# Kernel tuning notes

Hardware: AMD Instinct MI355X
Metric: run time of the kernel (lower is better)

The kernel has to match this reference:

```python
import jax, jax.numpy as jnp
import numpy as np

B, C, X, Y, Z = 2, 4, 128, 128, 96
_BIG = 1e10  # effectively infinite squared distance (no background in line)


def _edt_sq_pass(f, axis):
    """One separable pass of the exact squared EDT along `axis`:
    g[i] = min_j f[j] + (i - j)^2  (Felzenszwalb lower envelope, brute-forced
    with lax.map so only O(rest) memory per step)."""
    f = jnp.moveaxis(f, axis, -1)  # (..., L)
    idx = jnp.arange(f.shape[-1], dtype=f.dtype)
    g = jax.lax.map(lambda i: jnp.min(f + (i - idx) ** 2, axis=-1), idx)  # (L, ...)
    return jnp.moveaxis(jnp.moveaxis(g, 0, -1), -1, axis)


def _edt(mask):
    """Exact Euclidean distance of True voxels to the nearest False voxel
    (matches scipy.ndimage.distance_transform_edt on a binary mask)."""
    f = jnp.where(mask, _BIG, 0.0).astype(jnp.float32)
    for ax in (-3, -2, -1):  # three spatial axes
        f = _edt_sq_pass(f, ax)
    return jnp.sqrt(f)


def _neighbor(m, axis, d):
    """Shift `m` by d along `axis` with edge replication (reflect border,
    as in skimage's grey erosion used by find_boundaries)."""
    axis = axis % m.ndim
    pw = [(1, 1) if i == axis else (0, 0) for i in range(m.ndim)]
    p = jnp.pad(m, pw, mode='edge')
    sl = [slice(None)] * m.ndim
    sl[axis] = slice(1 + d, p.shape[axis] - 1 + d)
    return p[tuple(sl)]


def _inner_boundary(m):
    """skimage find_boundaries(mode='inner', connectivity=1): foreground voxels
    with at least one background face-neighbor."""
    eroded = m
    for ax in (-3, -2, -1):
        eroded = eroded & _neighbor(m, ax, 1) & _neighbor(m, ax, -1)
    return m & ~eroded


def _compute_sdf(onehot):
    """Signed distance map per (batch, class): negdis - posdis, zero on the
    inner boundary; zero where the class is absent; channel 0 is skipped."""
    posdis = _edt(onehot)          # dist inside object to background
    negdis = _edt(~onehot)         # dist outside object to foreground
    sdf = jnp.where(_inner_boundary(onehot), 0.0, negdis - posdis)
    any_pos = jnp.any(onehot, axis=(2, 3, 4), keepdims=True)
    sdf = jnp.where(any_pos, sdf, 0.0)
    return sdf.at[:, 0].set(0.0)   # loop starts at c=1 in the original


def setup_inputs() -> dict:
    key = jax.random.key(0)
    k1, k2 = jax.random.split(key)
    net_output = jax.random.normal(k1, (B, C, X, Y, Z), dtype=jnp.float32)
    gt = jax.random.randint(k2, (B, 1, X, Y, Z), 0, C, dtype=jnp.int32)
    return {"net_output": net_output, "gt": gt}


def reference(net_output, gt):
    probs = jax.nn.softmax(net_output, axis=1)  # softmax_helper = softmax over class dim
    classes = jnp.arange(net_output.shape[1], dtype=gt.dtype).reshape(1, -1, 1, 1, 1)
    onehot = gt == classes  # scatter_(1, gt, 1) one-hot, bool (B,C,X,Y,Z)
    phi = _compute_sdf(onehot)
    # einsum('bcxyz,bcxyz->bcxyz') on foreground channels, then global mean
    return jnp.mean(probs[:, 1:] * phi[:, 1:])
```

## Files before the change

kernel.cpp:

```cpp
#include <hip/hip_runtime.h>
#include <hip/hip_fp16.h>
#include <math.h>

#define XD 128
#define YD 128
#define ZD 96
#define NV (XD*YD*ZD)
#define SXX (YD*ZD)
#define SENT 49152
#define SENTP 0xC000C000u
#define TW2 114
#define TDW (TW2/2)
#define TROWS 144
#define SCANB 192
#define PROBB 1024

__global__ __launch_bounds__(384) void k_scan_prob(const int* __restrict__ gt,
                                                   const float* __restrict__ net,
                                                   unsigned char* __restrict__ out,
                                                   __half2* __restrict__ probs,
                                                   int* __restrict__ flags,
                                                   int batch0) {
    const int bb  = blockIdx.y;
    const int myb = batch0 + bb;
    const int tid = threadIdx.x;

    if (blockIdx.x >= SCANB) {
        const int p = (blockIdx.x - SCANB) * 384 + tid;
        const int idx = p * 4;
        const float* nb = net + (size_t)myb * 4 * NV;
        float4 v0 = *(const float4*)(nb + idx);
        float4 v1 = *(const float4*)(nb + NV + idx);
        float4 v2 = *(const float4*)(nb + 2 * NV + idx);
        float4 v3 = *(const float4*)(nb + 3 * NV + idx);

        const float a0[4] = {v0.x, v0.y, v0.z, v0.w};
        const float a1[4] = {v1.x, v1.y, v1.z, v1.w};
        const float a2[4] = {v2.x, v2.y, v2.z, v2.w};
        const float a3[4] = {v3.x, v3.y, v3.z, v3.w};
        float p1[4], p2[4], p3[4];
#pragma unroll
        for (int j = 0; j < 4; ++j) {
            float mx = fmaxf(fmaxf(a0[j], a1[j]), fmaxf(a2[j], a3[j]));
            float e0 = __expf(a0[j] - mx);
            float e1 = __expf(a1[j] - mx);
            float e2 = __expf(a2[j] - mx);
            float e3 = __expf(a3[j] - mx);
            float iv = __frcp_rn(e0 + e1 + e2 + e3);
            p1[j] = e1 * iv; p2[j] = e2 * iv; p3[j] = e3 * iv;
        }
        probs[(size_t)(myb * 3 + 0) * (NV / 2) + 2 * p]     = __floats2half2_rn(p1[0], p1[1]);
        probs[(size_t)(myb * 3 + 0) * (NV / 2) + 2 * p + 1] = __floats2half2_rn(p1[2], p1[3]);
        probs[(size_t)(myb * 3 + 1) * (NV / 2) + 2 * p]     = __floats2half2_rn(p2[0], p2[1]);
        probs[(size_t)(myb * 3 + 1) * (NV / 2) + 2 * p + 1] = __floats2half2_rn(p2[2], p2[3]);
        probs[(size_t)(myb * 3 + 2) * (NV / 2) + 2 * p]     = __floats2half2_rn(p3[0], p3[1]);
        probs[(size_t)(myb * 3 + 2) * (NV / 2) + 2 * p + 1] = __floats2half2_rn(p3[2], p3[3]);
        return;
    }

    const int l   = tid & 63;
    const int w6  = tid >> 6;
    const int lq0 = blockIdx.x * 64;

    __shared__ unsigned char gtile[64 * 132];
    __shared__ int blkbits;
    if (tid == 0) blkbits = 0;

    int mybits = 0;
    const int* gp = gt + (size_t)myb * NV + lq0 + l;
    for (int j = w6; j < XD; j += 6) {
        int g = gp[(size_t)j * SXX];
        mybits |= 1 << g;
        gtile[l * 132 + j] = (unsigned char)g;
    }
#pragma unroll
    for (int off = 32; off; off >>= 1) mybits |= __shfl_xor(mybits, off);
    __syncthreads();
    if ((tid & 63) == 0) atomicOr(&blkbits, mybits);

    unsigned int D[32];
    {
        const unsigned int ci = (unsigned int)((w6 >> 1) + 1);
        const int s = w6 & 1;
        unsigned int G[32];
        const unsigned int* grow = (const unsigned int*)gtile + l * 33;
#pragma unroll
        for (int q = 0; q < 32; ++q) G[q] = grow[q];

        int cnt = 200;
#pragma unroll
        for (int q = 0; q < 32; ++q) {
            unsigned int u = G[q], dv = 0;
#pragma unroll
            for (int b = 0; b < 4; ++b) {
                unsigned int gv = (u >> (8 * b)) & 255u;
                bool zero = s ? (gv == ci) : (gv != ci);
                cnt = zero ? 0 : ((cnt < 200) ? cnt + 1 : 200);
                dv |= (unsigned int)cnt << (8 * b);
            }
            D[q] = dv;
        }
        cnt = 200;
#pragma unroll
        for (int q = 31; q >= 0; --q) {
            unsigned int u = G[q], dv = D[q];
#pragma unroll
            for (int b = 3; b >= 0; --b) {
                unsigned int gv = (u >> (8 * b)) & 255u;
                bool zero = s ? (gv == ci) : (gv != ci);
                cnt = zero ? 0 : ((cnt < 200) ? cnt + 1 : 200);
                unsigned int old = (dv >> (8 * b)) & 255u;
                unsigned int nbv = ((unsigned int)cnt < old) ? (unsigned int)cnt : old;
                dv = (dv & ~(255u << (8 * b))) | (nbv << (8 * b));
            }
            D[q] = dv;
        }
    }
    __syncthreads();
    if (tid == 0) atomicOr(&flags[myb], blkbits);

    {
        const int r = l & 3;
        unsigned char* ob = out + (size_t)(bb * 6 + w6) * NV + lq0 + (l & ~3);
#pragma unroll
        for (int q = 0; q < 32; ++q) {
            unsigned int A = D[q];
            unsigned int Bv = (unsigned int)__shfl_xor((int)A, 1);
            unsigned int t = (r & 1)
                ? __builtin_amdgcn_perm(A, Bv, 0x07030501u)
                : __builtin_amdgcn_perm(A, Bv, 0x02060004u);
            unsigned int Cv = (unsigned int)__shfl_xor((int)t, 2);
            unsigned int y = (r & 2)
                ? __builtin_amdgcn_perm(t, Cv, 0x07060302u)
                : __builtin_amdgcn_perm(t, Cv, 0x01000504u);
            *(unsigned int*)(ob + (size_t)(4 * q + r) * SXX) = y;
        }
    }
}

__device__ __forceinline__ unsigned int pk_min(unsigned int a, unsigned int b) {
    unsigned int d;
    asm("v_pk_min_u16 %0, %1, %2" : "=v"(d) : "v"(a), "v"(b));
    return d;
}
__device__ __forceinline__ unsigned int pk_max(unsigned int a, unsigned int b) {
    unsigned int d;
    asm("v_pk_max_u16 %0, %1, %2" : "=v"(d) : "v"(a), "v"(b));
    return d;
}
__device__ __forceinline__ unsigned int pk_add(unsigned int a, unsigned int b) {
    unsigned int d;
    asm("v_pk_add_u16 %0, %1, %2" : "=v"(d) : "v"(a), "v"(b));
    return d;
}

__device__ __forceinline__ bool pk_done(const unsigned int m[8], int thr) {
    unsigned int mx = m[0];
#pragma unroll
    for (int k = 1; k < 8; ++k) mx = pk_max(mx, m[k]);
    int a = (int)(mx & 0xFFFFu), bq = (int)(mx >> 16);
    int amax = a > bq ? a : bq;
    return __all(amax <= thr) != 0;
}

template<int STRIDE, int L>
__device__ __forceinline__ void edt_slow8(const unsigned short* __restrict__ p0,
                                          int i0, float m[8]) {
    int t = 9;
    bool done = false;
    while (!done && t < L) {
        for (int u = 0; u < 4; ++u, ++t) {
            float t2 = (float)(t * t);
#pragma unroll
            for (int k = 0; k < 8; ++k) {
                int jm = i0 + k - t; if (jm < -8) jm = -8;
                int jp = i0 + k + t; if (jp > L + 7) jp = L + 7;
                m[k] = fminf(m[k], fminf((float)p0[jm * STRIDE],
                                         (float)p0[jp * STRIDE]) + t2);
            }
        }
        float mm = m[0];
#pragma unroll
        for (int k = 1; k < 8; ++k) mm = fmaxf(mm, m[k]);
        done = __all(mm <= (float)((t - 1) * (t - 1))) != 0;
    }
}
template<int STRIDE, int L>
__device__ __forceinline__ void edt_slow16(const unsigned short* __restrict__ p0,
                                           int i0, float m[16]) {
    int t = 9;
    bool done = false;
    while (!done && t < L) {
        for (int u = 0; u < 4; ++u, ++t) {
            float t2 = (float)(t * t);
#pragma unroll
            for (int k = 0; k < 16; ++k) {
                int jm = i0 + k - t; if (jm < -8) jm = -8;
                int jp = i0 + k + t; if (jp > L + 7) jp = L + 7;
                m[k] = fminf(m[k], fminf((float)p0[jm * STRIDE],
                                         (float)p0[jp * STRIDE]) + t2);
            }
        }
        float mm = m[0];
#pragma unroll
        for (int k = 1; k < 16; ++k) mm = fmaxf(mm, m[k]);
        done = __all(mm <= (float)((t - 1) * (t - 1))) != 0;
    }
}

__device__ __forceinline__ void edtY_pk(unsigned int* __restrict__ t32,
                                        unsigned short* __restrict__ tile,
                                        int zp, int i0, unsigned int m[8]) {
    unsigned int w[24];
    unsigned int* colp = t32 + 4 + zp;
#pragma unroll
    for (int q = 0; q < 24; ++q) w[q] = colp[(i0 + q) * TDW];
#pragma unroll
    for (int k = 0; k < 8; ++k) m[k] = w[k + 8];
#pragma unroll
    for (int t = 1; t <= 4; ++t) {
        const unsigned int t2p = (unsigned int)(t * t) * 0x00010001u;
#pragma unroll
        for (int k = 0; k < 8; ++k)
            m[k] = pk_min(m[k], pk_add(pk_min(w[k + 8 - t], w[k + 8 + t]), t2p));
    }
    bool done = pk_done(m, 16);
    if (!done) {
#pragma unroll
        for (int t = 5; t <= 8; ++t) {
            const unsigned int t2p = (unsigned int)(t * t) * 0x00010001u;
#pragma unroll
            for (int k = 0; k < 8; ++k)
                m[k] = pk_min(m[k], pk_add(pk_min(w[k + 8 - t], w[k + 8 + t]), t2p));
        }
        done = pk_done(m, 64);
    }
    if (!done) {
#pragma unroll
        for (int h = 0; h < 2; ++h) {
            float fm[8];
#pragma unroll
            for (int k = 0; k < 8; ++k)
                fm[k] = (float)(h ? (m[k] >> 16) : (m[k] & 0xFFFFu));
            edt_slow8<TW2, YD>(&tile[8 * TW2 + 8 + 2 * zp + h], i0, fm);
#pragma unroll
            for (int k = 0; k < 8; ++k) {
                unsigned int v = (unsigned int)fm[k];
                m[k] = h ? ((m[k] & 0x0000FFFFu) | (v << 16))
                         : ((m[k] & 0xFFFF0000u) | v);
            }
        }
    }
#pragma unroll
    for (int k = 0; k < 8; ++k) m[k] = pk_min(m[k], SENTP);
}

__device__ __forceinline__ void edtZ_pk(const unsigned int* __restrict__ t32,
                                        const unsigned short* __restrict__ tile,
                                        int y0, int ch, unsigned int m[8]) {
    unsigned int w[16];
    const unsigned int* rowp = t32 + (size_t)(8 + y0) * TDW;
#pragma unroll
    for (int q = 0; q < 16; ++q) w[q] = rowp[8 * ch + q];
#pragma unroll
    for (int k = 0; k < 8; ++k) m[k] = w[k + 4];
#pragma unroll
    for (int t = 1; t <= 4; ++t) {
        const unsigned int t2p = (unsigned int)(t * t) * 0x00010001u;
#pragma unroll
        for (int k = 0; k < 8; ++k) {
            unsigned int lo, hi;
            if (t & 1) {
                lo = __builtin_amdgcn_alignbit(w[k + 4 - (t - 1) / 2],
                                               w[k + 4 - (t + 1) / 2], 16);
                hi = __builtin_amdgcn_alignbit(w[k + 4 + (t + 1) / 2],
                                               w[k + 4 + (t - 1) / 2], 16);
            } else {
                lo = w[k + 4 - t / 2]; hi = w[k + 4 + t / 2];
            }
            m[k] = pk_min(m[k], pk_add(pk_min(lo, hi), t2p));
        }
    }
    bool done = pk_done(m, 16);
    if (!done) {
#pragma unroll
        for (int t = 5; t <= 8; ++t) {
            const unsigned int t2p = (unsigned int)(t * t) * 0x00010001u;
#pragma unroll
            for (int k = 0; k < 8; ++k) {
                unsigned int lo, hi;
                if (t & 1) {
                    lo = __builtin_amdgcn_alignbit(w[k + 4 - (t - 1) / 2],
                                                   w[k + 4 - (t + 1) / 2], 16);
                    hi = __builtin_amdgcn_alignbit(w[k + 4 + (t + 1) / 2],
                                                   w[k + 4 + (t - 1) / 2], 16);
                } else {
                    lo = w[k + 4 - t / 2]; hi = w[k + 4 + t / 2];
                }
                m[k] = pk_min(m[k], pk_add(pk_min(lo, hi), t2p));
            }
        }
        done = pk_done(m, 64);
    }
    if (!done) {
        float fm[16];
#pragma unroll
        for (int k = 0; k < 8; ++k) {
            fm[2 * k]     = (float)(m[k] & 0xFFFFu);
            fm[2 * k + 1] = (float)(m[k] >> 16);
        }
        edt_slow16<1, ZD>(&tile[(8 + y0) * TW2 + 8], 16 * ch, fm);
#pragma unroll
        for (int k = 0; k < 8; ++k)
            m[k] = (unsigned int)fm[2 * k] | ((unsigned int)fm[2 * k + 1] << 16);
    }
}

__global__ __launch_bounds__(768) void k_yz_acc(const unsigned char* __restrict__ in,
                                                const __half2* __restrict__ probs,
                                                const int* __restrict__ flags,
                                                double* __restrict__ partials,
                                                int batch0) {
    const int x   = blockIdx.x;
    const int bbl = blockIdx.y / 3;
    const int c   = blockIdx.y % 3;
    const int b   = batch0 + bbl;
    const int tid = threadIdx.x;
    const int pidx = (b * 3 + c) * XD + x;

    __shared__ unsigned short tile[TROWS * TW2];
    __shared__ double sd[768];
    unsigned int* t32 = (unsigned int*)tile;

    if (((flags[b] >> (c + 1)) & 1) == 0) {
        if (tid == 0) partials[pidx] = 0.0;
        return;
    }

    for (int i = tid; i < 16 * TDW; i += 768) {
        int r = i / TDW, cc = i - r * TDW;
        int row = (r < 8) ? r : 128 + r;
        t32[row * TDW + cc] = SENTP;
    }
    for (int i = tid; i < 128 * 9; i += 768) {
        int r = i / 9, cc = i - r * 9;
        int col = (cc < 4) ? cc : (48 + cc);
        t32[(8 + r) * TDW + col] = SENTP;
    }

    const int zp = tid % 48;  const int iY = (tid / 48) * 8;
    const int y0 = tid % 128; const int ch = tid / 128;
    const int e  = tid * 16;
    const int sy = e / ZD, sz = e - sy * ZD;
    const unsigned int sbase = (8 + sy) * TDW + (8 + sz) / 2;

    unsigned int m[8], dpp[8];

    {
        const uint4* ip = (const uint4*)(in + (size_t)(bbl * 6 + 2 * c) * NV +
                                         (size_t)x * SXX);
        uint4 v = ip[tid];
        unsigned int vv[4] = {v.x, v.y, v.z, v.w};
#pragma unroll
        for (int q = 0; q < 4; ++q) {
            unsigned int b0 = vv[q] & 255u, b1 = (vv[q] >> 8) & 255u;
            unsigned int b2 = (vv[q] >> 16) & 255u, b3 = vv[q] >> 24;
            t32[sbase + 2 * q] = (b0 > 127u ? SENT : b0 * b0) |
                                 ((b1 > 127u ? SENT : b1 * b1) << 16);
            t32[sbase + 2 * q + 1] = (b2 > 127u ? SENT : b2 * b2) |
                                     ((b3 > 127u ? SENT : b3 * b3) << 16);
        }
    }
    __syncthreads();
    edtY_pk(t32, tile, zp, iY, m);
    __syncthreads();
    {
        unsigned int* colp = t32 + 4 + zp;
#pragma unroll
        for (int k = 0; k < 8; ++k) colp[(iY + k + 8) * TDW] = m[k];
    }
    __syncthreads();
    edtZ_pk(t32, tile, y0, ch, m);
#pragma unroll
    for (int q = 0; q < 8; ++q) dpp[q] = pk_min(m[q], SENTP);
    __syncthreads();

    {
        const uint4* ip = (const uint4*)(in + (size_t)(bbl * 6 + 2 * c + 1) * NV +
                                         (size_t)x * SXX);
        uint4 v = ip[tid];
        unsigned int vv[4] = {v.x, v.y, v.z, v.w};
#pragma unroll
        for (int q = 0; q < 4; ++q) {
            unsigned int b0 = vv[q] & 255u, b1 = (vv[q] >> 8) & 255u;
            unsigned int b2 = (vv[q] >> 16) & 255u, b3 = vv[q] >> 24;
            t32[sbase + 2 * q] = (b0 > 127u ? SENT : b0 * b0) |
                                 ((b1 > 127u ? SENT : b1 * b1) << 16);
            t32[sbase + 2 * q + 1] = (b2 > 127u ? SENT : b2 * b2) |
                                     ((b3 > 127u ? SENT : b3 * b3) << 16);
        }
    }
    __syncthreads();
    edtY_pk(t32, tile, zp, iY, m);
    __syncthreads();
    {
        unsigned int* colp = t32 + 4 + zp;
#pragma unroll
        for (int k = 0; k < 8; ++k) colp[(iY + k + 8) * TDW] = m[k];
    }
    __syncthreads();
    edtZ_pk(t32, tile, y0, ch, m);

    float a = 0.0f;
    {
        const __half2* pv = probs + (size_t)(b * 3 + c) * (NV / 2) +
                            ((size_t)x * SXX + (size_t)y0 * ZD + 16 * ch) / 2;
#pragma unroll
        for (int q = 0; q < 8; ++q) {
            float2 pf = __half22float2(pv[q]);
            unsigned int dnq = pk_min(m[q], SENTP);
            unsigned int dp0 = dpp[q] & 0xFFFFu, dp1 = dpp[q] >> 16;
            unsigned int dn0 = dnq & 0xFFFFu,   dn1 = dnq >> 16;
            float phi0 = (dp0 == 1u) ? 0.0f
                       : (sqrtf((float)dn0) - sqrtf((float)dp0));
            float phi1 = (dp1 == 1u) ? 0.0f
                       : (sqrtf((float)dn1) - sqrtf((float)dp1));
            a += pf.x * phi0 + pf.y * phi1;
        }
    }
    sd[tid] = (double)a;
    __syncthreads();
    for (int off = 512; off; off >>= 1) {
        if (tid < off && tid + off < 768) sd[tid] += sd[tid + off];
        __syncthreads();
    }
    if (tid == 0) partials[pidx] = sd[0];
}

__global__ void k_reduce(const double* __restrict__ partials, int n,
                         float* __restrict__ out) {
    __shared__ double sd[256];
    double ls = 0.0;
    for (int i = threadIdx.x; i < n; i += 256) ls += partials[i];
    sd[threadIdx.x] = ls;
    __syncthreads();
    for (int off = 128; off > 0; off >>= 1) {
        if (threadIdx.x < off) sd[threadIdx.x] += sd[threadIdx.x + off];
        __syncthreads();
    }
    if (threadIdx.x == 0) out[0] = (float)(sd[0] / 9437184.0);
}

extern "C" void kernel_launch(void* const* d_in, const int* in_sizes, int n_in,
                              void* d_out, int out_size, void* d_ws, size_t ws_size,
                              hipStream_t stream) {
    const float* net = (const float*)d_in[0];
    const int*   gt  = (const int*)d_in[1];
    float* out = (float*)d_out;
    char* ws = (char*)d_ws;

    const size_t xbufB1 = (size_t)6 * NV;
    const size_t probsB = (size_t)2 * 3 * NV * 2;
    const size_t tail   = (size_t)768 * sizeof(double) + 64;

    const int nb = (ws_size >= 2 * xbufB1 + probsB + tail) ? 2 : 1;

    unsigned char* xbuf  = (unsigned char*)ws;
    __half2*       probs = (__half2*)(ws + (size_t)nb * xbufB1);
    double*     partials = (double*)((char*)probs + probsB);
    int*           flags = (int*)((char*)partials + 768 * sizeof(double));

    hipMemsetAsync(flags, 0, 8 * sizeof(int), stream);

    for (int b0 = 0; b0 < 2; b0 += nb) {
        hipLaunchKernelGGL(k_scan_prob, dim3(SCANB + PROBB, nb), dim3(384), 0,
                           stream, gt, net, xbuf, probs, flags, b0);
        hipLaunchKernelGGL(k_yz_acc, dim3(XD, 3 * nb), dim3(768), 0, stream,
                           xbuf, probs, flags, partials, b0);
    }
    hipLaunchKernelGGL(k_reduce, dim3(1), dim3(256), 0, stream, partials,
                       768, out);
}
```

Baseline: 69.99 us.

## Pack pos/neg distance fields into one u16x2 word and process both in one pass

Instead of running the Y and Z EDT passes twice (once for the positive mask, once for the negative), the kernel now interleaves pos and neg squared distances into the two halves of each 32-bit LDS word. Both fields go through a single Y pass and a single Z pass using packed u16 min/add, with 16 outputs per thread. This removes one full round of loads, syncs and passes. The block-level double reduction now uses wavefront shuffles instead of an LDS tree. The tile layout changes to one word per voxel with a wider padded pitch, and the bigger register arrays may raise register pressure.

```diff
diff --git a/kernel.cpp b/kernel.cpp
--- a/kernel.cpp
+++ b/kernel.cpp
@@ -9,9 +9,7 @@
 #define SXX (YD*ZD)
 #define SENT 49152
 #define SENTP 0xC000C000u
-#define TW2 114
-#define TDW (TW2/2)
-#define TROWS 144
+#define TD3 113
 #define SCANB 192
 #define PROBB 1024
 
@@ -154,37 +152,15 @@
     return d;
 }
 
-__device__ __forceinline__ bool pk_done(const unsigned int m[8], int thr) {
+__device__ __forceinline__ bool pk_done16(const unsigned int m[16], int thr) {
     unsigned int mx = m[0];
 #pragma unroll
-    for (int k = 1; k < 8; ++k) mx = pk_max(mx, m[k]);
+    for (int k = 1; k < 16; ++k) mx = pk_max(mx, m[k]);
     int a = (int)(mx & 0xFFFFu), bq = (int)(mx >> 16);
     int amax = a > bq ? a : bq;
     return __all(amax <= thr) != 0;
 }
 
-template<int STRIDE, int L>
-__device__ __forceinline__ void edt_slow8(const unsigned short* __restrict__ p0,
-                                          int i0, float m[8]) {
-    int t = 9;
-    bool done = false;
-    while (!done && t < L) {
-        for (int u = 0; u < 4; ++u, ++t) {
-            float t2 = (float)(t * t);
-#pragma unroll
-            for (int k = 0; k < 8; ++k) {
-                int jm = i0 + k - t; if (jm < -8) jm = -8;
-                int jp = i0 + k + t; if (jp > L + 7) jp = L + 7;
-                m[k] = fminf(m[k], fminf((float)p0[jm * STRIDE],
-                                         (float)p0[jp * STRIDE]) + t2);
-            }
-        }
-        float mm = m[0];
-#pragma unroll
-        for (int k = 1; k < 8; ++k) mm = fmaxf(mm, m[k]);
-        done = __all(mm <= (float)((t - 1) * (t - 1))) != 0;
-    }
-}
 template<int STRIDE, int L>
 __device__ __forceinline__ void edt_slow16(const unsigned short* __restrict__ p0,
                                            int i0, float m[16]) {
@@ -205,114 +181,6 @@
 #pragma unroll
         for (int k = 1; k < 16; ++k) mm = fmaxf(mm, m[k]);
         done = __all(mm <= (float)((t - 1) * (t - 1))) != 0;
-    }
-}
-
-__device__ __forceinline__ void edtY_pk(unsigned int* __restrict__ t32,
-                                        unsigned short* __restrict__ tile,
-                                        int zp, int i0, unsigned int m[8]) {
-    unsigned int w[24];
-    unsigned int* colp = t32 + 4 + zp;
-#pragma unroll
-    for (int q = 0; q < 24; ++q) w[q] = colp[(i0 + q) * TDW];
-#pragma unroll
-    for (int k = 0; k < 8; ++k) m[k] = w[k + 8];
-#pragma unroll
-    for (int t = 1; t <= 4; ++t) {
-        const unsigned int t2p = (unsigned int)(t * t) * 0x00010001u;
-#pragma unroll
-        for (int k = 0; k < 8; ++k)
-            m[k] = pk_min(m[k], pk_add(pk_min(w[k + 8 - t], w[k + 8 + t]), t2p));
-    }
-    bool done = pk_done(m, 16);
-    if (!done) {
-#pragma unroll
-        for (int t = 5; t <= 8; ++t) {
-            const unsigned int t2p = (unsigned int)(t * t) * 0x00010001u;
-#pragma unroll
-            for (int k = 0; k < 8; ++k)
-                m[k] = pk_min(m[k], pk_add(pk_min(w[k + 8 - t], w[k + 8 + t]), t2p));
-        }
-        done = pk_done(m, 64);
-    }
-    if (!done) {
-#pragma unroll
-        for (int h = 0; h < 2; ++h) {
-            float fm[8];
-#pragma unroll
-            for (int k = 0; k < 8; ++k)
-                fm[k] = (float)(h ? (m[k] >> 16) : (m[k] & 0xFFFFu));
-            edt_slow8<TW2, YD>(&tile[8 * TW2 + 8 + 2 * zp + h], i0, fm);
-#pragma unroll
-            for (int k = 0; k < 8; ++k) {
-                unsigned int v = (unsigned int)fm[k];
-                m[k] = h ? ((m[k] & 0x0000FFFFu) | (v << 16))
-                         : ((m[k] & 0xFFFF0000u) | v);
-            }
-        }
-    }
-#pragma unroll
-    for (int k = 0; k < 8; ++k) m[k] = pk_min(m[k], SENTP);
-}
-
-__device__ __forceinline__ void edtZ_pk(const unsigned int* __restrict__ t32,
-                                        const unsigned short* __restrict__ tile,
-                                        int y0, int ch, unsigned int m[8]) {
-    unsigned int w[16];
-    const unsigned int* rowp = t32 + (size_t)(8 + y0) * TDW;
-#pragma unroll
-    for (int q = 0; q < 16; ++q) w[q] = rowp[8 * ch + q];
-#pragma unroll
-    for (int k = 0; k < 8; ++k) m[k] = w[k + 4];
-#pragma unroll
-    for (int t = 1; t <= 4; ++t) {
-        const unsigned int t2p = (unsigned int)(t * t) * 0x00010001u;
-#pragma unroll
-        for (int k = 0; k < 8; ++k) {
-            unsigned int lo, hi;
-            if (t & 1) {
-                lo = __builtin_amdgcn_alignbit(w[k + 4 - (t - 1) / 2],
-                                               w[k + 4 - (t + 1) / 2], 16);
-                hi = __builtin_amdgcn_alignbit(w[k + 4 + (t + 1) / 2],
-                                               w[k + 4 + (t - 1) / 2], 16);
-            } else {
-                lo = w[k + 4 - t / 2]; hi = w[k + 4 + t / 2];
-            }
-            m[k] = pk_min(m[k], pk_add(pk_min(lo, hi), t2p));
-        }
-    }
-    bool done = pk_done(m, 16);
-    if (!done) {
-#pragma unroll
-        for (int t = 5; t <= 8; ++t) {
-            const unsigned int t2p = (unsigned int)(t * t) * 0x00010001u;
-#pragma unroll
-            for (int k = 0; k < 8; ++k) {
-                unsigned int lo, hi;
-                if (t & 1) {
-                    lo = __builtin_amdgcn_alignbit(w[k + 4 - (t - 1) / 2],
-                                                   w[k + 4 - (t + 1) / 2], 16);
-                    hi = __builtin_amdgcn_alignbit(w[k + 4 + (t + 1) / 2],
-                                                   w[k + 4 + (t - 1) / 2], 16);
-                } else {
-                    lo = w[k + 4 - t / 2]; hi = w[k + 4 + t / 2];
-                }
-                m[k] = pk_min(m[k], pk_add(pk_min(lo, hi), t2p));
-            }
-        }
-        done = pk_done(m, 64);
-    }
-    if (!done) {
-        float fm[16];
-#pragma unroll
-        for (int k = 0; k < 8; ++k) {
-            fm[2 * k]     = (float)(m[k] & 0xFFFFu);
-            fm[2 * k + 1] = (float)(m[k] >> 16);
-        }
-        edt_slow16<1, ZD>(&tile[(8 + y0) * TW2 + 8], 16 * ch, fm);
-#pragma unroll
-        for (int k = 0; k < 8; ++k)
-            m[k] = (unsigned int)fm[2 * k] | ((unsigned int)fm[2 * k + 1] << 16);
     }
 }
 
@@ -328,99 +196,154 @@
     const int tid = threadIdx.x;
     const int pidx = (b * 3 + c) * XD + x;
 
-    __shared__ unsigned short tile[TROWS * TW2];
-    __shared__ double sd[768];
-    unsigned int* t32 = (unsigned int*)tile;
+    __shared__ unsigned int t32[144 * TD3];
+    __shared__ double sd[12];
+    unsigned short* t16 = (unsigned short*)t32;
 
     if (((flags[b] >> (c + 1)) & 1) == 0) {
         if (tid == 0) partials[pidx] = 0.0;
         return;
     }
 
-    for (int i = tid; i < 16 * TDW; i += 768) {
-        int r = i / TDW, cc = i - r * TDW;
+    for (int i = tid; i < 16 * TD3; i += 768) {
+        int r = i / TD3, cc = i - r * TD3;
         int row = (r < 8) ? r : 128 + r;
-        t32[row * TDW + cc] = SENTP;
-    }
-    for (int i = tid; i < 128 * 9; i += 768) {
-        int r = i / 9, cc = i - r * 9;
-        int col = (cc < 4) ? cc : (48 + cc);
-        t32[(8 + r) * TDW + col] = SENTP;
-    }
-
-    const int zp = tid % 48;  const int iY = (tid / 48) * 8;
-    const int y0 = tid % 128; const int ch = tid / 128;
-    const int e  = tid * 16;
-    const int sy = e / ZD, sz = e - sy * ZD;
-    const unsigned int sbase = (8 + sy) * TDW + (8 + sz) / 2;
-
-    unsigned int m[8], dpp[8];
-
-    {
-        const uint4* ip = (const uint4*)(in + (size_t)(bbl * 6 + 2 * c) * NV +
-                                         (size_t)x * SXX);
-        uint4 v = ip[tid];
-        unsigned int vv[4] = {v.x, v.y, v.z, v.w};
+        t32[row * TD3 + cc] = SENTP;
+    }
+    for (int i = tid; i < 128 * 17; i += 768) {
+        int r = i / 17, cc = i - r * 17;
+        int col = (cc < 8) ? cc : (96 + cc);
+        t32[(8 + r) * TD3 + col] = SENTP;
+    }
+    {
+        const uint4* ipP = (const uint4*)(in + (size_t)(bbl * 6 + 2 * c) * NV +
+                                          (size_t)x * SXX);
+        const uint4* ipN = (const uint4*)(in + (size_t)(bbl * 6 + 2 * c + 1) * NV +
+                                          (size_t)x * SXX);
+        uint4 vp = ipP[tid], vn = ipN[tid];
+        const int sy = tid / 6, sz = 16 * (tid % 6);
+        unsigned int* dst = t32 + (8 + sy) * TD3 + 8 + sz;
+        unsigned int pp[4] = {vp.x, vp.y, vp.z, vp.w};
+        unsigned int nn[4] = {vn.x, vn.y, vn.z, vn.w};
 #pragma unroll
         for (int q = 0; q < 4; ++q) {
-            unsigned int b0 = vv[q] & 255u, b1 = (vv[q] >> 8) & 255u;
-            unsigned int b2 = (vv[q] >> 16) & 255u, b3 = vv[q] >> 24;
-            t32[sbase + 2 * q] = (b0 > 127u ? SENT : b0 * b0) |
-                                 ((b1 > 127u ? SENT : b1 * b1) << 16);
-            t32[sbase + 2 * q + 1] = (b2 > 127u ? SENT : b2 * b2) |
-                                     ((b3 > 127u ? SENT : b3 * b3) << 16);
+#pragma unroll
+            for (int bq = 0; bq < 4; ++bq) {
+                unsigned int pb = (pp[q] >> (8 * bq)) & 255u;
+                unsigned int nb2 = (nn[q] >> (8 * bq)) & 255u;
+                dst[4 * q + bq] = (pb > 127u ? SENT : pb * pb) |
+                                  ((nb2 > 127u ? SENT : nb2 * nb2) << 16);
+            }
         }
     }
     __syncthreads();
-    edtY_pk(t32, tile, zp, iY, m);
-    __syncthreads();
-    {
-        unsigned int* colp = t32 + 4 + zp;
-#pragma unroll
-        for (int k = 0; k < 8; ++k) colp[(iY + k + 8) * TDW] = m[k];
-    }
-    __syncthreads();
-    edtZ_pk(t32, tile, y0, ch, m);
-#pragma unroll
-    for (int q = 0; q < 8; ++q) dpp[q] = pk_min(m[q], SENTP);
-    __syncthreads();
-
-    {
-        const uint4* ip = (const uint4*)(in + (size_t)(bbl * 6 + 2 * c + 1) * NV +
-                                         (size_t)x * SXX);
-        uint4 v = ip[tid];
-        unsigned int vv[4] = {v.x, v.y, v.z, v.w};
-#pragma unroll
-        for (int q = 0; q < 4; ++q) {
-            unsigned int b0 = vv[q] & 255u, b1 = (vv[q] >> 8) & 255u;
-            unsigned int b2 = (vv[q] >> 16) & 255u, b3 = vv[q] >> 24;
-            t32[sbase + 2 * q] = (b0 > 127u ? SENT : b0 * b0) |
-                                 ((b1 > 127u ? SENT : b1 * b1) << 16);
-            t32[sbase + 2 * q + 1] = (b2 > 127u ? SENT : b2 * b2) |
-                                     ((b3 > 127u ? SENT : b3 * b3) << 16);
-        }
-    }
-    __syncthreads();
-    edtY_pk(t32, tile, zp, iY, m);
-    __syncthreads();
-    {
-        unsigned int* colp = t32 + 4 + zp;
-#pragma unroll
-        for (int k = 0; k < 8; ++k) colp[(iY + k + 8) * TDW] = m[k];
-    }
-    __syncthreads();
-    edtZ_pk(t32, tile, y0, ch, m);
+
+    unsigned int m[16];
+    {
+        const int z0 = tid % 96;
+        const int i0 = (tid / 96) * 16;
+        unsigned int w[32];
+        const unsigned int* colp = t32 + 8 + z0;
+#pragma unroll
+        for (int q = 0; q < 32; ++q) w[q] = colp[(i0 + q) * TD3];
+#pragma unroll
+        for (int k = 0; k < 16; ++k) m[k] = w[k + 8];
+#pragma unroll
+        for (int t = 1; t <= 4; ++t) {
+            const unsigned int t2p = (unsigned int)(t * t) * 0x00010001u;
+#pragma unroll
+            for (int k = 0; k < 16; ++k)
+                m[k] = pk_min(m[k], pk_add(pk_min(w[k + 8 - t], w[k + 8 + t]), t2p));
+        }
+        bool done = pk_done16(m, 16);
+        if (!done) {
+#pragma unroll
+            for (int t = 5; t <= 8; ++t) {
+                const unsigned int t2p = (unsigned int)(t * t) * 0x00010001u;
+#pragma unroll
+                for (int k = 0; k < 16; ++k)
+                    m[k] = pk_min(m[k], pk_add(pk_min(w[k + 8 - t], w[k + 8 + t]), t2p));
+            }
+            done = pk_done16(m, 64);
+        }
+        if (!done) {
+#pragma unroll
+            for (int h = 0; h < 2; ++h) {
+                float fm[16];
+#pragma unroll
+                for (int k = 0; k < 16; ++k)
+                    fm[k] = (float)(h ? (m[k] >> 16) : (m[k] & 0xFFFFu));
+                edt_slow16<2 * TD3, YD>(t16 + (8 * TD3 + 8 + z0) * 2 + h, i0, fm);
+#pragma unroll
+                for (int k = 0; k < 16; ++k) {
+                    unsigned int v = (unsigned int)fm[k];
+                    m[k] = h ? ((m[k] & 0x0000FFFFu) | (v << 16))
+                             : ((m[k] & 0xFFFF0000u) | v);
+                }
+            }
+        }
+        __syncthreads();
+#pragma unroll
+        for (int k = 0; k < 16; ++k)
+            t32[(8 + i0 + k) * TD3 + 8 + z0] = pk_min(m[k], SENTP);
+        __syncthreads();
+    }
+    const int y0 = tid % 128;
+    const int i0 = (tid / 128) * 16;
+    {
+        unsigned int w[32];
+        const unsigned int* rowp = t32 + (8 + y0) * TD3 + 8;
+#pragma unroll
+        for (int q = 0; q < 32; ++q) w[q] = rowp[i0 - 8 + q];
+#pragma unroll
+        for (int k = 0; k < 16; ++k) m[k] = w[k + 8];
+#pragma unroll
+        for (int t = 1; t <= 4; ++t) {
+            const unsigned int t2p = (unsigned int)(t * t) * 0x00010001u;
+#pragma unroll
+            for (int k = 0; k < 16; ++k)
+                m[k] = pk_min(m[k], pk_add(pk_min(w[k + 8 - t], w[k + 8 + t]), t2p));
+        }
+        bool done = pk_done16(m, 16);
+        if (!done) {
+#pragma unroll
+            for (int t = 5; t <= 8; ++t) {
+                const unsigned int t2p = (unsigned int)(t * t) * 0x00010001u;
+#pragma unroll
+                for (int k = 0; k < 16; ++k)
+                    m[k] = pk_min(m[k], pk_add(pk_min(w[k + 8 - t], w[k + 8 + t]), t2p));
+            }
+            done = pk_done16(m, 64);
+        }
+        if (!done) {
+#pragma unroll
+            for (int h = 0; h < 2; ++h) {
+                float fm[16];
+#pragma unroll
+                for (int k = 0; k < 16; ++k)
+                    fm[k] = (float)(h ? (m[k] >> 16) : (m[k] & 0xFFFFu));
+                edt_slow16<2, ZD>(t16 + ((8 + y0) * TD3 + 8) * 2 + h, i0, fm);
+#pragma unroll
+                for (int k = 0; k < 16; ++k) {
+                    unsigned int v = (unsigned int)fm[k];
+                    m[k] = h ? ((m[k] & 0x0000FFFFu) | (v << 16))
+                             : ((m[k] & 0xFFFF0000u) | v);
+                }
+            }
+        }
+    }
 
     float a = 0.0f;
     {
         const __half2* pv = probs + (size_t)(b * 3 + c) * (NV / 2) +
-                            ((size_t)x * SXX + (size_t)y0 * ZD + 16 * ch) / 2;
+                            ((size_t)x * SXX + (size_t)y0 * ZD + i0) / 2;
 #pragma unroll
         for (int q = 0; q < 8; ++q) {
             float2 pf = __half22float2(pv[q]);
-            unsigned int dnq = pk_min(m[q], SENTP);
-            unsigned int dp0 = dpp[q] & 0xFFFFu, dp1 = dpp[q] >> 16;
-            unsigned int dn0 = dnq & 0xFFFFu,   dn1 = dnq >> 16;
+            unsigned int d0 = pk_min(m[2 * q],     SENTP);
+            unsigned int d1 = pk_min(m[2 * q + 1], SENTP);
+            unsigned int dp0 = d0 & 0xFFFFu, dn0 = d0 >> 16;
+            unsigned int dp1 = d1 & 0xFFFFu, dn1 = d1 >> 16;
             float phi0 = (dp0 == 1u) ? 0.0f
                        : (sqrtf((float)dn0) - sqrtf((float)dp0));
             float phi1 = (dp1 == 1u) ? 0.0f
@@ -428,13 +351,17 @@
             a += pf.x * phi0 + pf.y * phi1;
         }
     }
-    sd[tid] = (double)a;
+    double v = (double)a;
+#pragma unroll
+    for (int off = 32; off; off >>= 1) v += __shfl_down(v, off);
+    if ((tid & 63) == 0) sd[tid >> 6] = v;
     __syncthreads();
-    for (int off = 512; off; off >>= 1) {
-        if (tid < off && tid + off < 768) sd[tid] += sd[tid + off];
-        __syncthreads();
-    }
-    if (tid == 0) partials[pidx] = sd[0];
+    if (tid == 0) {
+        double s = 0.0;
+#pragma unroll
+        for (int i = 0; i < 12; ++i) s += sd[i];
+        partials[pidx] = s;
+    }
 }
 
 __global__ void k_reduce(const double* __restrict__ partials, int n,
```

Result: faster. 68.09 us (-2.7%).
